# Kernel optimization log

Measured on AMD Instinct MI355X. Metric: run time of the kernel, lower is better.

The kernel has to match this reference:

```python
import jax, jax.numpy as jnp
import numpy as np

DIM = 128        # per-head dim == model width in this module
Q_HEADS = 16
KV_HEADS = 4
WINDOW = 512
BATCH = 4
SEQ = 2048


def setup_inputs() -> dict:
    key = jax.random.key(0)
    k1, k2, k3 = jax.random.split(key, 3)
    x = jax.random.normal(k1, (BATCH, SEQ, DIM), dtype=jnp.float32)
    # fused qkv weight, stored (in, out) so forward is x @ W_qkv
    W_qkv = jax.random.normal(k2, (DIM, (Q_HEADS + 2 * KV_HEADS) * DIM), dtype=jnp.float32) * (DIM ** -0.5)
    W_proj = jax.random.normal(k3, (Q_HEADS * DIM, DIM), dtype=jnp.float32) * ((Q_HEADS * DIM) ** -0.5)
    return {"x": x, "W_qkv": W_qkv, "W_proj": W_proj}


def _gqa_forward(x, W_qkv, W_proj):
    b, s, d = x.shape
    qkv = x @ W_qkv                                    # [b, s, (Hq+2Hkv)*d]
    qkv = qkv.reshape(b, s, Q_HEADS + 2 * KV_HEADS, d).transpose(0, 2, 1, 3)
    q = qkv[:, :Q_HEADS]                               # [b, Hq, s, d]
    k = qkv[:, Q_HEADS:Q_HEADS + KV_HEADS]             # [b, Hkv, s, d]
    v = qkv[:, Q_HEADS + KV_HEADS:]                    # [b, Hkv, s, d]

    # GQA: repeat kv heads to match q heads
    group = Q_HEADS // KV_HEADS
    k = jnp.repeat(k, group, axis=1)                   # [b, Hq, s, d]
    v = jnp.repeat(v, group, axis=1)

    scale = 1.0 / jnp.sqrt(jnp.float32(d))
    scores = jnp.einsum('bhqd,bhkd->bhqk', q, k) * scale   # [b, Hq, s, s]

    q_idx = jnp.arange(s)[:, None]
    kv_idx = jnp.arange(s)[None, :]
    rel = (q_idx - kv_idx).astype(jnp.float32)         # [s, s]
    # per-head ALiBi slope: exp2(-(h+1)*8/Hq), added (sign matches source)
    h = jnp.arange(Q_HEADS, dtype=jnp.float32)
    slopes = jnp.exp2(-((h + 1.0) * 8.0 / Q_HEADS))    # [Hq]
    scores = scores + slopes[None, :, None, None] * rel[None, None, :, :]

    mask = (q_idx >= kv_idx) & ((q_idx - kv_idx) <= WINDOW)
    scores = jnp.where(mask[None, None], scores, -jnp.inf)
    probs = jax.nn.softmax(scores, axis=-1)

    att = jnp.einsum('bhqk,bhkd->bhqd', probs, v)      # [b, Hq, s, d]
    att = att.transpose(0, 2, 1, 3).reshape(b, s, Q_HEADS * d)
    return att @ W_proj                                # [b, s, d]


def reference(x, W_qkv, W_proj):
    return _gqa_forward(x, W_qkv, W_proj)
```

## Files before the change

kernel.cpp:

```cpp
#include <hip/hip_runtime.h>
#include <math.h>

#define DIM_    128
#define QH_     16
#define KVH_    4
#define WIN_    512
#define BATCH_  4
#define SEQ_    2048
#define QKV_LD  3072
#define ATT_LD  2048

#define NX   (BATCH_*SEQ_*DIM_)
#define NWQ  (DIM_*QKV_LD)
#define NWP  (ATT_LD*DIM_)

typedef __attribute__((ext_vector_type(8))) short short8;
typedef __attribute__((ext_vector_type(4))) float f32x4;
typedef unsigned short u16;
typedef unsigned int u32;

__device__ __forceinline__ u16 f2bf(float f) {
    u32 u = __float_as_uint(f);
    u += 0x7fff + ((u >> 16) & 1);
    return (u16)(u >> 16);
}
__device__ __forceinline__ float bf2f(u16 u) {
    return __uint_as_float(((u32)u) << 16);
}
#define MFMA16 __builtin_amdgcn_mfma_f32_16x16x32_bf16

#if __has_builtin(__builtin_amdgcn_exp2f)
#define EXP2F __builtin_amdgcn_exp2f
#else
#define EXP2F exp2f
#endif

__device__ __forceinline__ void gload_lds16(const u16* g, u16* l) {
    __builtin_amdgcn_global_load_lds(
        (const __attribute__((address_space(1))) unsigned int*)(const void*)g,
        (__attribute__((address_space(3))) unsigned int*)(void*)l, 16, 0, 0);
}

__global__ __launch_bounds__(256) void xcvt(
    const float* __restrict__ x, u16* __restrict__ xh)
{
    const size_t t = (size_t)blockIdx.x * 256 + threadIdx.x;
    float4 v = *(const float4*)(x + 4 * t);
    ushort4 o;
    o.x = f2bf(v.x); o.y = f2bf(v.y); o.z = f2bf(v.z); o.w = f2bf(v.w);
    *(ushort4*)(xh + 4 * t) = o;
}

__global__ __launch_bounds__(256) void wtrans(
    const float* __restrict__ Wqkv, const float* __restrict__ Wproj,
    u16* __restrict__ wth, u16* __restrict__ wpth)
{
    __shared__ float T[32][33];
    int tile = blockIdx.x;
    const float* src; u16* dst; int K, N;
    if (tile < 384) { src = Wqkv;  dst = wth;  K = 128;  N = 3072; }
    else { tile -= 384; src = Wproj; dst = wpth; K = 2048; N = 128; }
    const int ntile = N >> 5;
    const int k0 = (tile / ntile) << 5, n0 = (tile % ntile) << 5;
    const int tx = threadIdx.x & 31, ty = threadIdx.x >> 5;
    #pragma unroll
    for (int i = 0; i < 4; ++i)
        T[ty + 8 * i][tx] = src[(size_t)(k0 + ty + 8 * i) * N + n0 + tx];
    __syncthreads();
    #pragma unroll
    for (int i = 0; i < 4; ++i)
        dst[(size_t)(n0 + ty + 8 * i) * K + k0 + tx] = f2bf(T[tx][ty + 8 * i]);
}

__global__ __launch_bounds__(256) void gemm1_mfma(
    const u16* __restrict__ xh, const u16* __restrict__ wth,
    u16* __restrict__ qkvb, u16* __restrict__ vg)
{
    __shared__ u16 Ab[32][512];
    __shared__ u16 Bb[16][512];
    const int bn = blockIdx.x * 64;
    const int bm = blockIdx.y * 128;
    const int tid = threadIdx.x;
    const int wv = tid >> 6, lane = tid & 63;
    const int lr = lane & 15, quad = lane >> 4;
    const int lo = lane & 15, hi = lane >> 4;

    #pragma unroll
    for (int i = 0; i < 12; ++i) {
        const int idx = wv * 12 + i;
        if (idx < 32) {
            const int mt = idx >> 2, s = idx & 3;
            gload_lds16(xh + (size_t)(bm + mt * 16 + lo) * DIM_ + s * 32 + hi * 8,
                        &Ab[idx][0]);
        } else {
            const int j = idx - 32, nt = j >> 2, s = j & 3;
            gload_lds16(wth + (size_t)(bn + nt * 16 + lo) * DIM_ + s * 32 + hi * 8,
                        &Bb[j][0]);
        }
    }
    __syncthreads();

    const int wr = wv >> 1, wc = wv & 1;
    f32x4 acc[4][2] = {};
    if (bn < 2560) {
        #pragma unroll
        for (int s = 0; s < 4; ++s) {
            short8 af[4], bf[2];
            #pragma unroll
            for (int mt = 0; mt < 4; ++mt)
                af[mt] = *(const short8*)&Ab[(wr * 4 + mt) * 4 + s][lane * 8];
            #pragma unroll
            for (int nt = 0; nt < 2; ++nt)
                bf[nt] = *(const short8*)&Bb[(wc * 2 + nt) * 4 + s][lane * 8];
            #pragma unroll
            for (int mt = 0; mt < 4; ++mt)
                #pragma unroll
                for (int nt = 0; nt < 2; ++nt)
                    acc[mt][nt] = MFMA16(bf[nt], af[mt], acc[mt][nt], 0, 0, 0);
        }
        #pragma unroll
        for (int mt = 0; mt < 4; ++mt)
            #pragma unroll
            for (int nt = 0; nt < 2; ++nt) {
                ushort4 o;
                o.x = f2bf(acc[mt][nt][0]); o.y = f2bf(acc[mt][nt][1]);
                o.z = f2bf(acc[mt][nt][2]); o.w = f2bf(acc[mt][nt][3]);
                *(ushort4*)(qkvb
                    + (size_t)(bm + wr * 64 + mt * 16 + lr) * QKV_LD
                    + bn + wc * 32 + nt * 16 + quad * 4) = o;
            }
    } else {
        #pragma unroll
        for (int s = 0; s < 4; ++s) {
            short8 af[4], bf[2];
            #pragma unroll
            for (int mt = 0; mt < 4; ++mt)
                af[mt] = *(const short8*)&Ab[(wr * 4 + mt) * 4 + s][lane * 8];
            #pragma unroll
            for (int nt = 0; nt < 2; ++nt)
                bf[nt] = *(const short8*)&Bb[(wc * 2 + nt) * 4 + s][lane * 8];
            #pragma unroll
            for (int mt = 0; mt < 4; ++mt)
                #pragma unroll
                for (int nt = 0; nt < 2; ++nt)
                    acc[mt][nt] = MFMA16(af[mt], bf[nt], acc[mt][nt], 0, 0, 0);
        }
        #pragma unroll
        for (int mt = 0; mt < 4; ++mt)
            #pragma unroll
            for (int nt = 0; nt < 2; ++nt) {
                const int ncol = bn + wc * 32 + nt * 16 + lr - 2560;
                const int kvh = ncol >> 7, d = ncol & 127;
                const int m0 = bm + wr * 64 + mt * 16 + quad * 4;
                ushort4 o;
                o.x = f2bf(acc[mt][nt][0]); o.y = f2bf(acc[mt][nt][1]);
                o.z = f2bf(acc[mt][nt][2]); o.w = f2bf(acc[mt][nt][3]);
                *(ushort4*)(vg + ((size_t)((m0 >> 11) * KVH_ + kvh) * DIM_ + d)
                            * SEQ_ + (m0 & 2047)) = o;
            }
    }
}

__global__ __launch_bounds__(256) void attn_mfma(
    const u16* __restrict__ qkvb, const u16* __restrict__ vg,
    u16* __restrict__ ah)
{
    const int qt = blockIdx.x, kvh = blockIdx.y, b = blockIdx.z;
    const int q0 = qt << 5;
    const int tid = threadIdx.x;
    const int wv = tid >> 6, lane = tid & 63;
    const int lr = lane & 15, quad = lane >> 4;
    const int h = kvh * 4 + wv;

    __shared__ u16 Kb[4][8][512];
    __shared__ u16 Vb[4][8][512];
    __shared__ u16 Pt[4][32][36];

    const float scale2 = 0.08838834764831845f * 1.4426950408889634f;
    const float slope2 = exp2f(-0.5f * (float)(h + 1)) * 1.4426950408889634f;
    const int jbase = max(0, q0 - WIN_);
    const int nch = (q0 + 32 - jbase) >> 5;
    const size_t rowb = (size_t)b * SEQ_;
    const u16* kg  = qkvb + rowb * QKV_LD + (QH_ + kvh) * DIM_;
    const u16* vgb = vg + (size_t)(b * KVH_ + kvh) * DIM_ * SEQ_;
    const int lo = lane & 15, hi = lane >> 4;

    short8 qf[2][4];
    #pragma unroll
    for (int m = 0; m < 2; ++m) {
        const u16* qp = qkvb + (rowb + q0 + m * 16 + lr) * QKV_LD
                        + h * DIM_ + quad * 8;
        #pragma unroll
        for (int s = 0; s < 4; ++s) qf[m][s] = *(const short8*)(qp + 32 * s);
    }

    float alpha[2];
    #pragma unroll
    for (int m = 0; m < 2; ++m) {
        const int q = q0 + m * 16 + lr;
        const int rm = (q < WIN_) ? q : WIN_;
        alpha[m] = slope2 * (float)(q - rm);
    }

    f32x4 O[2][8] = {};
    float rs[2] = {0.f, 0.f};

    #define STAGE(CH, SLOT) do {                                              \
        const int _jk = jbase + ((CH) << 5);                                  \
        _Pragma("unroll")                                                     \
        for (int _t = 0; _t < 2; ++_t) {                                      \
            const int _p = wv + _t * 4;                                       \
            gload_lds16(kg + (size_t)(_jk + (_p >> 2) * 16 + lo) * QKV_LD     \
                        + (_p & 3) * 32 + hi * 8, &Kb[(SLOT)][_p][0]);        \
            gload_lds16(vgb + (size_t)(_p * 16 + lo) * SEQ_ + _jk + hi * 8,   \
                        &Vb[(SLOT)][_p][0]);                                  \
        }                                                                     \
    } while (0)

    STAGE(0, 0);
    { const int c1 = (1 < nch) ? 1 : (nch - 1); STAGE(c1, 1); }

    for (int ch = 0; ch < nch; ++ch) {
        const int jk = jbase + (ch << 5);
        const int slot = ch & 3;
        { const int cn = (ch + 2 < nch) ? (ch + 2) : (nch - 1);
          STAGE(cn, (ch + 2) & 3); }
        __asm__ volatile("s_waitcnt vmcnt(8)" ::: "memory");
        __asm__ volatile("s_barrier" ::: "memory");

        #pragma unroll
        for (int nt = 0; nt < 2; ++nt) {
            f32x4 c0 = {0.f, 0.f, 0.f, 0.f}, c1 = {0.f, 0.f, 0.f, 0.f};
            #pragma unroll
            for (int s = 0; s < 4; ++s) {
                short8 kf = *(const short8*)&Kb[slot][nt * 4 + s][lane * 8];
                c0 = MFMA16(kf, qf[0][s], c0, 0, 0, 0);
                c1 = MFMA16(kf, qf[1][s], c1, 0, 0, 0);
            }
            const int jknt = jk + nt * 16;
            #pragma unroll
            for (int m = 0; m < 2; ++m) {
                const f32x4 c = m ? c1 : c0;
                const int qm0 = q0 + m * 16;
                const float b0 = fmaf(-slope2, (float)(jknt + quad * 4), alpha[m]);
                float e0, e1, e2, e3;
                if (qm0 >= jknt + 15 && qm0 + 15 <= jknt + WIN_) {
                    e0 = EXP2F(fmaf(c[0], scale2, b0));
                    e1 = EXP2F(fmaf(c[1], scale2, b0 - slope2));
                    e2 = EXP2F(fmaf(c[2], scale2, b0 - 2.f * slope2));
                    e3 = EXP2F(fmaf(c[3], scale2, b0 - 3.f * slope2));
                } else {
                    const int q = qm0 + lr, j0q = jknt + quad * 4;
                    float ee[4];
                    #pragma unroll
                    for (int r = 0; r < 4; ++r) {
                        const int rel = q - (j0q + r);
                        const float t = fmaf(c[r], scale2, b0 - (float)r * slope2);
                        ee[r] = ((unsigned)rel <= (unsigned)WIN_) ? EXP2F(t) : 0.f;
                    }
                    e0 = ee[0]; e1 = ee[1]; e2 = ee[2]; e3 = ee[3];
                }
                rs[m] += (e0 + e1) + (e2 + e3);
                ushort4 o;
                o.x = f2bf(e0); o.y = f2bf(e1); o.z = f2bf(e2); o.w = f2bf(e3);
                *(ushort4*)&Pt[wv][m * 16 + lr][nt * 16 + quad * 4] = o;
            }
        }
        __asm__ volatile("s_waitcnt lgkmcnt(0)" ::: "memory");

        short8 pa0 = *(const short8*)&Pt[wv][lr][quad * 8];
        short8 pa1 = *(const short8*)&Pt[wv][16 + lr][quad * 8];
        #pragma unroll
        for (int nt = 0; nt < 8; ++nt) {
            short8 vf = *(const short8*)&Vb[slot][nt][lane * 8];
            O[0][nt] = MFMA16(vf, pa0, O[0][nt], 0, 0, 0);
            O[1][nt] = MFMA16(vf, pa1, O[1][nt], 0, 0, 0);
        }
    }
    #undef STAGE

    __asm__ volatile("s_waitcnt vmcnt(0)" ::: "memory");

    #pragma unroll
    for (int m = 0; m < 2; ++m) {
        rs[m] += __shfl_xor(rs[m], 16);
        rs[m] += __shfl_xor(rs[m], 32);
    }

    #pragma unroll
    for (int m = 0; m < 2; ++m) {
        const float inv = 1.0f / rs[m];
        u16* dst = ah + (rowb + q0 + m * 16 + lr) * (size_t)ATT_LD + h * DIM_;
        #pragma unroll
        for (int nt = 0; nt < 8; ++nt) {
            ushort4 o;
            o.x = f2bf(O[m][nt][0] * inv); o.y = f2bf(O[m][nt][1] * inv);
            o.z = f2bf(O[m][nt][2] * inv); o.w = f2bf(O[m][nt][3] * inv);
            *(ushort4*)(dst + nt * 16 + quad * 4) = o;
        }
    }
}

__global__ __launch_bounds__(256) void gemm2_mfma(
    const u16* __restrict__ ah, const u16* __restrict__ wpth,
    float* __restrict__ out)
{
    const int bm = blockIdx.x * 16;
    const int wv = threadIdx.x >> 6, lane = threadIdx.x & 63;
    const int lr = lane & 15, quad = lane >> 4;
    const int cq = wv;

    const u16* arow  = ah + (size_t)(bm + lr) * ATT_LD + quad * 8;
    const u16* w0row = wpth + (size_t)(cq * 32 + lr) * ATT_LD + quad * 8;
    const u16* w1row = w0row + (size_t)16 * ATT_LD;

    f32x4 acc0 = {0.f, 0.f, 0.f, 0.f}, acc1 = {0.f, 0.f, 0.f, 0.f};
    #pragma unroll 8
    for (int k0 = 0; k0 < ATT_LD; k0 += 32) {
        short8 a  = *(const short8*)(arow + k0);
        short8 w0 = *(const short8*)(w0row + k0);
        short8 w1 = *(const short8*)(w1row + k0);
        acc0 = MFMA16(w0, a, acc0, 0, 0, 0);
        acc1 = MFMA16(w1, a, acc1, 0, 0, 0);
    }
    float* orow = out + (size_t)(bm + lr) * DIM_ + cq * 32;
    *(float4*)(orow + quad * 4)      = *(float4*)&acc0;
    *(float4*)(orow + 16 + quad * 4) = *(float4*)&acc1;
}

extern "C" void kernel_launch(void* const* d_in, const int* in_sizes, int n_in,
                              void* d_out, int out_size, void* d_ws, size_t ws_size,
                              hipStream_t stream)
{
    const float* x     = (const float*)d_in[0];
    const float* Wqkv  = (const float*)d_in[1];
    const float* Wproj = (const float*)d_in[2];
    float* out = (float*)d_out;

    u16* xh   = (u16*)d_ws;
    u16* wth  = xh   + (size_t)NX;
    u16* wpth = wth  + (size_t)NWQ;
    u16* qkvb = wpth + (size_t)NWP;
    u16* vg   = qkvb + (size_t)8192 * QKV_LD;
    u16* ahp  = vg   + (size_t)BATCH_ * KVH_ * DIM_ * SEQ_;

    xcvt<<<NX / 1024, 256, 0, stream>>>(x, xh);
    wtrans<<<384 + 256, 256, 0, stream>>>(Wqkv, Wproj, wth, wpth);

    gemm1_mfma<<<dim3(QKV_LD / 64, 8192 / 128), 256, 0, stream>>>(
        xh, wth, qkvb, vg);

    attn_mfma<<<dim3(SEQ_ / 32, KVH_, BATCH_), 256, 0, stream>>>(qkvb, vg, ahp);

    gemm2_mfma<<<8192 / 16, 256, 0, stream>>>(ahp, wpth, out);
}
```

Measured before the change: 207.9 us.

## Merge prep kernels and restructure attention K/V prefetch with single barrier

Folds the x conversion and weight-transpose kernels into one launch to save a kernel launch. In the attention kernel, K and V staging are split: K is triple-buffered two chunks ahead and V double-buffered one chunk ahead, with prefetches issued after the barrier so a single barrier protects buffer reuse. This shrinks LDS usage, which may raise occupancy, but gives V loads less lead time.

```diff
diff --git a/kernel.cpp b/kernel.cpp
--- a/kernel.cpp
+++ b/kernel.cpp
@@ -41,22 +41,21 @@
         (__attribute__((address_space(3))) unsigned int*)(void*)l, 16, 0, 0);
 }
 
-__global__ __launch_bounds__(256) void xcvt(
-    const float* __restrict__ x, u16* __restrict__ xh)
-{
-    const size_t t = (size_t)blockIdx.x * 256 + threadIdx.x;
-    float4 v = *(const float4*)(x + 4 * t);
-    ushort4 o;
-    o.x = f2bf(v.x); o.y = f2bf(v.y); o.z = f2bf(v.z); o.w = f2bf(v.w);
-    *(ushort4*)(xh + 4 * t) = o;
-}
-
-__global__ __launch_bounds__(256) void wtrans(
-    const float* __restrict__ Wqkv, const float* __restrict__ Wproj,
-    u16* __restrict__ wth, u16* __restrict__ wpth)
-{
+__global__ __launch_bounds__(256) void prep(
+    const float* __restrict__ x, const float* __restrict__ Wqkv,
+    const float* __restrict__ Wproj,
+    u16* __restrict__ xh, u16* __restrict__ wth, u16* __restrict__ wpth)
+{
+    if (blockIdx.x < 1024) {
+        const size_t t = (size_t)blockIdx.x * 256 + threadIdx.x;
+        float4 v = *(const float4*)(x + 4 * t);
+        ushort4 o;
+        o.x = f2bf(v.x); o.y = f2bf(v.y); o.z = f2bf(v.z); o.w = f2bf(v.w);
+        *(ushort4*)(xh + 4 * t) = o;
+        return;
+    }
     __shared__ float T[32][33];
-    int tile = blockIdx.x;
+    int tile = blockIdx.x - 1024;
     const float* src; u16* dst; int K, N;
     if (tile < 384) { src = Wqkv;  dst = wth;  K = 128;  N = 3072; }
     else { tile -= 384; src = Wproj; dst = wpth; K = 2048; N = 128; }
@@ -172,8 +171,8 @@
     const int lr = lane & 15, quad = lane >> 4;
     const int h = kvh * 4 + wv;
 
-    __shared__ u16 Kb[4][8][512];
-    __shared__ u16 Vb[4][8][512];
+    __shared__ u16 Kb[3][8][512];
+    __shared__ u16 Vb[2][8][512];
     __shared__ u16 Pt[4][32][36];
 
     const float scale2 = 0.08838834764831845f * 1.4426950408889634f;
@@ -205,35 +204,45 @@
     f32x4 O[2][8] = {};
     float rs[2] = {0.f, 0.f};
 
-    #define STAGE(CH, SLOT) do {                                              \
+    #define STAGE_K(CH, SLOT) do {                                            \
         const int _jk = jbase + ((CH) << 5);                                  \
         _Pragma("unroll")                                                     \
         for (int _t = 0; _t < 2; ++_t) {                                      \
             const int _p = wv + _t * 4;                                       \
             gload_lds16(kg + (size_t)(_jk + (_p >> 2) * 16 + lo) * QKV_LD     \
                         + (_p & 3) * 32 + hi * 8, &Kb[(SLOT)][_p][0]);        \
-            gload_lds16(vgb + (size_t)(_p * 16 + lo) * SEQ_ + _jk + hi * 8,   \
+        }                                                                     \
+    } while (0)
+    #define STAGE_V(CH, SLOT) do {                                            \
+        const int _jv = jbase + ((CH) << 5);                                  \
+        _Pragma("unroll")                                                     \
+        for (int _t = 0; _t < 2; ++_t) {                                      \
+            const int _p = wv + _t * 4;                                       \
+            gload_lds16(vgb + (size_t)(_p * 16 + lo) * SEQ_ + _jv + hi * 8,   \
                         &Vb[(SLOT)][_p][0]);                                  \
         }                                                                     \
     } while (0)
 
-    STAGE(0, 0);
-    { const int c1 = (1 < nch) ? 1 : (nch - 1); STAGE(c1, 1); }
+    STAGE_K(0, 0);
+    STAGE_V(0, 0);
+    { const int c1 = (1 < nch) ? 1 : 0; STAGE_K(c1, 1); }
 
     for (int ch = 0; ch < nch; ++ch) {
         const int jk = jbase + (ch << 5);
-        const int slot = ch & 3;
-        { const int cn = (ch + 2 < nch) ? (ch + 2) : (nch - 1);
-          STAGE(cn, (ch + 2) & 3); }
-        __asm__ volatile("s_waitcnt vmcnt(8)" ::: "memory");
+        const int ks = ch % 3, vs = ch & 1;
+        __asm__ volatile("s_waitcnt vmcnt(2)" ::: "memory");
         __asm__ volatile("s_barrier" ::: "memory");
+        { const int vc = (ch + 1 < nch) ? ch + 1 : nch - 1;
+          STAGE_V(vc, (ch + 1) & 1); }
+        { const int kc = (ch + 2 < nch) ? ch + 2 : nch - 1;
+          STAGE_K(kc, (ch + 2) % 3); }
 
         #pragma unroll
         for (int nt = 0; nt < 2; ++nt) {
             f32x4 c0 = {0.f, 0.f, 0.f, 0.f}, c1 = {0.f, 0.f, 0.f, 0.f};
             #pragma unroll
             for (int s = 0; s < 4; ++s) {
-                short8 kf = *(const short8*)&Kb[slot][nt * 4 + s][lane * 8];
+                short8 kf = *(const short8*)&Kb[ks][nt * 4 + s][lane * 8];
                 c0 = MFMA16(kf, qf[0][s], c0, 0, 0, 0);
                 c1 = MFMA16(kf, qf[1][s], c1, 0, 0, 0);
             }
@@ -272,12 +281,13 @@
         short8 pa1 = *(const short8*)&Pt[wv][16 + lr][quad * 8];
         #pragma unroll
         for (int nt = 0; nt < 8; ++nt) {
-            short8 vf = *(const short8*)&Vb[slot][nt][lane * 8];
+            short8 vf = *(const short8*)&Vb[vs][nt][lane * 8];
             O[0][nt] = MFMA16(vf, pa0, O[0][nt], 0, 0, 0);
             O[1][nt] = MFMA16(vf, pa1, O[1][nt], 0, 0, 0);
         }
     }
-    #undef STAGE
+    #undef STAGE_K
+    #undef STAGE_V
 
     __asm__ volatile("s_waitcnt vmcnt(0)" ::: "memory");
 
@@ -344,8 +354,7 @@
     u16* vg   = qkvb + (size_t)8192 * QKV_LD;
     u16* ahp  = vg   + (size_t)BATCH_ * KVH_ * DIM_ * SEQ_;
 
-    xcvt<<<NX / 1024, 256, 0, stream>>>(x, xh);
-    wtrans<<<384 + 256, 256, 0, stream>>>(Wqkv, Wproj, wth, wpth);
+    prep<<<1024 + 640, 256, 0, stream>>>(x, Wqkv, Wproj, xh, wth, wpth);
 
     gemm1_mfma<<<dim3(QKV_LD / 64, 8192 / 128), 256, 0, stream>>>(
         xh, wth, qkvb, vg);
```

After: 210.7 us. Within noise of the previous version (+1.3%).
